# Kernel optimization log

Measured on AMD Instinct MI355X. Metric: run time of the kernel, lower is better.

## Reference

```python
import jax, jax.numpy as jnp
import numpy as np

# Fixed module configuration (matches init_kwargs)
B, T, H, W, C = 2, 16, 32, 32, 512
NH, DH = 8, 64          # num_heads, head_dim = C // NH
MLP = 2048
EPS = 1e-6              # flax LayerNorm default epsilon


def _xavier(key, shape):
    fan_in, fan_out = shape[-2], shape[-1]
    lim = np.sqrt(6.0 / (fan_in + fan_out)).astype(np.float32)
    return jax.random.uniform(key, shape, jnp.float32, -lim, lim)


def setup_inputs() -> dict:
    key = jax.random.key(0)
    ks = jax.random.split(key, 8)
    return {
        "x": jax.random.normal(ks[0], (B, T * H * W, C), jnp.float32),
        # per-axis (stacked: 0=time, 1=height, 2=width) attention params
        "ln_scale": jnp.ones((3, C), jnp.float32),
        "ln_bias": jnp.zeros((3, C), jnp.float32),
        "wq": _xavier(ks[1], (3, C, C)), "bq": jnp.zeros((3, C), jnp.float32),
        "wk": _xavier(ks[2], (3, C, C)), "bk": jnp.zeros((3, C), jnp.float32),
        "wv": _xavier(ks[3], (3, C, C)), "bv": jnp.zeros((3, C), jnp.float32),
        "wo": _xavier(ks[4], (3, C, C)), "bo": jnp.zeros((3, C), jnp.float32),
        # final LN + MLP params
        "ln_mlp_scale": jnp.ones((C,), jnp.float32),
        "ln_mlp_bias": jnp.zeros((C,), jnp.float32),
        "w1": _xavier(ks[5], (C, MLP)),
        "b1": jax.random.normal(ks[6], (MLP,), jnp.float32) * 1e-6,
        "w2": _xavier(ks[7], (MLP, C)),
        "b2": jnp.zeros((C,), jnp.float32),
    }


def _ln(x, scale, bias):
    m = jnp.mean(x, axis=-1, keepdims=True)
    v = jnp.var(x, axis=-1, keepdims=True)
    return (x - m) * jax.lax.rsqrt(v + EPS) * scale + bias


def _mha(x, wq, bq, wk, bk, wv, bv, wo, bo):
    # x: [Bf, S, C]; standard flax-style MHA (query scaled by 1/sqrt(head_dim))
    Bf, S, _ = x.shape
    q = (x @ wq + bq).reshape(Bf, S, NH, DH) * (1.0 / np.sqrt(DH).astype(np.float32))
    k = (x @ wk + bk).reshape(Bf, S, NH, DH)
    v = (x @ wv + bv).reshape(Bf, S, NH, DH)
    a = jax.nn.softmax(jnp.einsum('bqhd,bkhd->bhqk', q, k), axis=-1)
    o = jnp.einsum('bhqk,bkhd->bqhd', a, v).reshape(Bf, S, C)
    return o @ wo + bo


def _axial(x5, axis, sc, bi, wq, bq, wk, bk, wv, bv, wo, bo):
    # fold all non-`axis` spatial dims into batch, attend along `axis`
    other = [a for a in (1, 2, 3) if a != axis]
    perm = [0] + other + [axis, 4]
    xp = jnp.transpose(x5, perm)                      # [..., S_axis, C]
    pshape = xp.shape
    x1 = xp.reshape(-1, pshape[-2], C)                # [Bf, S_axis, C]
    y = _mha(_ln(x1, sc, bi), wq, bq, wk, bk, wv, bv, wo, bo) + x1  # pre-LN residual
    y = y.reshape(pshape)
    inv = list(np.argsort(perm))
    return jnp.transpose(y, inv)


def reference(x, ln_scale, ln_bias, wq, bq, wk, bk, wv, bv, wo, bo,
              ln_mlp_scale, ln_mlp_bias, w1, b1, w2, b2):
    x5 = x.reshape(B, T, H, W, C)
    for i, axis in enumerate((1, 2, 3)):  # time, height, width
        x5 = _axial(x5, axis, ln_scale[i], ln_bias[i], wq[i], bq[i],
                    wk[i], bk[i], wv[i], bv[i], wo[i], bo[i])
    xf = x5.reshape(B, T * H * W, C)
    y = _ln(xf, ln_mlp_scale, ln_mlp_bias)
    y = jax.nn.gelu(y @ w1 + b1) @ w2 + b2            # gelu approximate=True (flax default)
    return xf + y
```

## Files before the change

### kernel.cpp

```cpp
#include <hip/hip_runtime.h>
#include <hip/hip_bf16.h>

typedef __attribute__((ext_vector_type(8))) short short8;
typedef __attribute__((ext_vector_type(4))) float f32x4;

static __device__ __forceinline__ short f2bf(float f) {
    union { __hip_bfloat16 h; short s; } u;
    u.h = __float2bfloat16(f);
    return u.s;
}

static __device__ __forceinline__ float gelu_tanh(float v) {
    const float c = 0.7978845608028654f;
    float t = tanhf(c * (v + 0.044715f * v * v * v));
    return 0.5f * v * (1.f + t);
}

__global__ __launch_bounds__(256) void cvt_weights(
    const float* __restrict__ wq, const float* __restrict__ wk,
    const float* __restrict__ wv, const float* __restrict__ wo,
    const float* __restrict__ w1, const float* __restrict__ w2,
    short* __restrict__ wT)
{
    const long NSQ = 12L * 262144;
    long gid = (long)blockIdx.x * 256 + threadIdx.x;
    if (gid < NSQ) {
        int m = (int)(gid >> 18);
        int rem = (int)(gid & 262143);
        int n = rem >> 9, k = rem & 511;
        int a = m >> 2, t = m & 3;
        const float* src = (t == 0) ? wq : (t == 1) ? wk : (t == 2) ? wv : wo;
        wT[gid] = f2bf(src[(long)a * 262144 + (long)k * 512 + n]);
    } else if (gid < NSQ + 1048576) {
        int r = (int)(gid - NSQ);
        int n = r >> 9, k = r & 511;
        wT[gid] = f2bf(w1[(long)k * 2048 + n]);
    } else {
        int r = (int)(gid - NSQ - 1048576);
        int n = r >> 11, k = r & 2047;
        wT[gid] = f2bf(w2[(long)k * 512 + n]);
    }
}

__global__ __launch_bounds__(256) void ln_kernel(
    const float* __restrict__ x, const float* __restrict__ sc,
    const float* __restrict__ bi, short* __restrict__ out)
{
    int row = blockIdx.x * 4 + (threadIdx.x >> 6);
    int lane = threadIdx.x & 63;
    const float* xr = x + (long)row * 512 + lane * 8;
    f32x4 v0 = *(const f32x4*)xr;
    f32x4 v1 = *(const f32x4*)(xr + 4);
    float s = 0.f, ss = 0.f;
#pragma unroll
    for (int i = 0; i < 4; i++) { s += v0[i] + v1[i]; ss += v0[i] * v0[i] + v1[i] * v1[i]; }
#pragma unroll
    for (int m = 1; m < 64; m <<= 1) { s += __shfl_xor(s, m, 64); ss += __shfl_xor(ss, m, 64); }
    float mean = s * (1.f / 512.f);
    float var  = ss * (1.f / 512.f) - mean * mean;
    float rs = rsqrtf(var + 1e-6f);
    f32x4 s0 = *(const f32x4*)(sc + lane * 8);
    f32x4 s1 = *(const f32x4*)(sc + lane * 8 + 4);
    f32x4 b0 = *(const f32x4*)(bi + lane * 8);
    f32x4 b1 = *(const f32x4*)(bi + lane * 8 + 4);
    short8 o;
#pragma unroll
    for (int i = 0; i < 4; i++) o[i]     = f2bf((v0[i] - mean) * rs * s0[i] + b0[i]);
#pragma unroll
    for (int i = 0; i < 4; i++) o[4 + i] = f2bf((v1[i] - mean) * rs * s1[i] + b1[i]);
    *(short8*)(out + (long)row * 512 + lane * 8) = o;
}

template<int EPI>
__global__ __launch_bounds__(256, 2) void gemm_nt(
    const short* __restrict__ A, const short* __restrict__ Bt,
    const float* __restrict__ bias, const float* __restrict__ bias2,
    const float* __restrict__ bias3,
    const float* __restrict__ res, float* __restrict__ outf,
    short* __restrict__ outb, int M, int N, int K, float scale)
{
    __shared__ __align__(16) short As[128 * 64];
    __shared__ __align__(16) short Bs[128 * 64];
    const int t = threadIdx.x;
    const int lane = t & 63, wid = t >> 6;
    const int wm = wid >> 1, wn = wid & 1;
    const int m0 = blockIdx.x * 128, n0 = blockIdx.y * 128;

    const short* Ag = A  + (long)m0 * K;
    const short* Bg = Bt + (long)n0 * K;

    f32x4 acc[4][4];
#pragma unroll
    for (int i = 0; i < 4; i++)
#pragma unroll
        for (int j = 0; j < 4; j++) acc[i][j] = (f32x4){0.f, 0.f, 0.f, 0.f};

    short8 areg[4], breg[4];
#pragma unroll
    for (int c = 0; c < 4; c++) {
        int g = c * 256 + t; int r = g >> 3, kc = g & 7;
        areg[c] = *(const short8*)(Ag + (long)r * K + kc * 8);
        breg[c] = *(const short8*)(Bg + (long)r * K + kc * 8);
    }
    const int NT = K >> 6;
    for (int tt = 0; tt < NT; ++tt) {
#pragma unroll
        for (int c = 0; c < 4; c++) {
            int g = c * 256 + t; int r = g >> 3, kc = g & 7;
            int off = r * 128 + ((kc * 16) ^ ((r & 7) << 4));
            *(short8*)((char*)As + off) = areg[c];
            *(short8*)((char*)Bs + off) = breg[c];
        }
        __syncthreads();
        if (tt + 1 < NT) {
            const short* Ag2 = Ag + (tt + 1) * 64;
            const short* Bg2 = Bg + (tt + 1) * 64;
#pragma unroll
            for (int c = 0; c < 4; c++) {
                int g = c * 256 + t; int r = g >> 3, kc = g & 7;
                areg[c] = *(const short8*)(Ag2 + (long)r * K + kc * 8);
                breg[c] = *(const short8*)(Bg2 + (long)r * K + kc * 8);
            }
        }
        const int arow = wm * 64 + (lane & 15);
        const int brow = wn * 64 + (lane & 15);
        const int kb = (lane >> 4) * 16;
#pragma unroll
        for (int ks = 0; ks < 2; ++ks) {
            short8 af[4], bfr[4];
#pragma unroll
            for (int f = 0; f < 4; f++) {
                int ra = arow + f * 16;
                af[f]  = *(short8*)((char*)As + ra * 128 + ((kb + ks * 64) ^ ((ra & 7) << 4)));
                int rb = brow + f * 16;
                bfr[f] = *(short8*)((char*)Bs + rb * 128 + ((kb + ks * 64) ^ ((rb & 7) << 4)));
            }
#pragma unroll
            for (int i = 0; i < 4; i++)
#pragma unroll
                for (int j = 0; j < 4; j++)
                    acc[i][j] = __builtin_amdgcn_mfma_f32_16x16x32_bf16(af[i], bfr[j], acc[i][j], 0, 0, 0);
        }
        __syncthreads();
    }

#pragma unroll
    for (int j = 0; j < 4; j++) {
        int col = n0 + wn * 64 + j * 16 + (lane & 15);
        float bv;
        float sc_part = 1.f;
        if (EPI == 3) {
            int part = col >> 9;
            const float* bp = (part == 0) ? bias : (part == 1) ? bias2 : bias3;
            bv = bp[col & 511];
            if (part == 0) sc_part = scale;
        } else {
            bv = bias[col];
        }
#pragma unroll
        for (int i = 0; i < 4; i++) {
            int row0 = m0 + wm * 64 + i * 16 + ((lane >> 4) << 2);
#pragma unroll
            for (int r = 0; r < 4; r++) {
                int row = row0 + r;
                long idx = (long)row * N + col;
                float v = acc[i][j][r] + bv;
                if (EPI == 1)      outf[idx] = v + res[idx];
                else if (EPI == 2) outb[idx] = f2bf(gelu_tanh(v));
                else               outb[idx] = f2bf(v * sc_part);
            }
        }
    }
}

template<int S, int PASS>
__global__ __launch_bounds__(64) void attn_kernel(
    const short* __restrict__ Q, const short* __restrict__ Kx,
    const short* __restrict__ V, short* __restrict__ O, int ld)
{
    constexpr int MF = S / 16;
    constexpr int SP = 32;
    __shared__ __align__(16) short P_lds[S * SP];
    __shared__ __align__(16) short Vt[64 * SP];

    const int lane = threadIdx.x;
    const int pair = blockIdx.x;
    const int head = pair & 7;
    const int bf = pair >> 3;
    long base; int stride;
    if (PASS == 0)      { base = (long)(bf >> 10) * 16384 + (bf & 1023); stride = 1024; }
    else if (PASS == 1) { int b = bf >> 9, t = (bf >> 5) & 15, w = bf & 31; base = (long)b * 16384 + t * 1024 + w; stride = 32; }
    else                { int b = bf >> 9, t = (bf >> 5) & 15, h = bf & 31; base = (long)b * 16384 + t * 1024 + (h << 5); stride = 1; }
    const int hoff = head * 64;

    if (S == 16) {
        short8 z = {0, 0, 0, 0, 0, 0, 0, 0};
        *(short8*)(P_lds + lane * 8) = z;
#pragma unroll
        for (int i = 0; i < 4; i++) *(short8*)(Vt + lane * 32 + i * 8) = z;
        __syncthreads();
    }

    short8 qf[MF][2], kf[MF][2];
#pragma unroll
    for (int f = 0; f < MF; f++) {
        int r = f * 16 + (lane & 15);
        const short* qp = Q + (base + (long)r * stride) * ld + hoff + ((lane >> 4) * 8);
        qf[f][0] = *(const short8*)qp;
        qf[f][1] = *(const short8*)(qp + 32);
        const short* kp = Kx + (base + (long)r * stride) * ld + hoff + ((lane >> 4) * 8);
        kf[f][0] = *(const short8*)kp;
        kf[f][1] = *(const short8*)(kp + 32);
    }

    short8 vv[4];
    const int vr  = (S == 32) ? (lane & 31) : (lane & 15);
    const int vd0 = (S == 32) ? ((lane >> 5) * 32) : ((lane >> 4) * 16);
    constexpr int NVC = (S == 32) ? 4 : 2;
    {
        const short* vp = V + (base + (long)vr * stride) * ld + hoff + vd0;
#pragma unroll
        for (int c = 0; c < NVC; c++) vv[c] = *(const short8*)(vp + c * 8);
    }
#pragma unroll
    for (int c = 0; c < NVC; c++)
#pragma unroll
        for (int e = 0; e < 8; e++)
            Vt[(vd0 + c * 8 + e) * SP + vr] = vv[c][e];

    f32x4 zero4 = {0.f, 0.f, 0.f, 0.f};
    f32x4 sc[MF][MF];
#pragma unroll
    for (int i = 0; i < MF; i++)
#pragma unroll
        for (int j = 0; j < MF; j++) {
            f32x4 a = __builtin_amdgcn_mfma_f32_16x16x32_bf16(qf[i][0], kf[j][0], zero4, 0, 0, 0);
            sc[i][j] = __builtin_amdgcn_mfma_f32_16x16x32_bf16(qf[i][1], kf[j][1], a, 0, 0, 0);
        }

#pragma unroll
    for (int i = 0; i < MF; i++) {
#pragma unroll
        for (int r = 0; r < 4; r++) {
            float mx = sc[i][0][r];
            if (MF == 2) mx = fmaxf(mx, sc[i][1][r]);
#pragma unroll
            for (int m = 1; m < 16; m <<= 1) mx = fmaxf(mx, __shfl_xor(mx, m, 64));
            float e0 = expf(sc[i][0][r] - mx);
            float e1 = (MF == 2) ? expf(sc[i][1][r] - mx) : 0.f;
            float sum = e0 + e1;
#pragma unroll
            for (int m = 1; m < 16; m <<= 1) sum += __shfl_xor(sum, m, 64);
            float inv = 1.f / sum;
            int row = i * 16 + ((lane >> 4) << 2) + r;
            P_lds[row * SP + (lane & 15)] = f2bf(e0 * inv);
            if (MF == 2) P_lds[row * SP + 16 + (lane & 15)] = f2bf(e1 * inv);
        }
    }
    __syncthreads();

    short8 pa[MF];
#pragma unroll
    for (int f = 0; f < MF; f++)
        pa[f] = *(const short8*)(P_lds + (f * 16 + (lane & 15)) * SP + (lane >> 4) * 8);
    short8 vbf[4];
#pragma unroll
    for (int n = 0; n < 4; n++)
        vbf[n] = *(const short8*)(Vt + (n * 16 + (lane & 15)) * SP + (lane >> 4) * 8);
    f32x4 of[MF][4];
#pragma unroll
    for (int f = 0; f < MF; f++)
#pragma unroll
        for (int n = 0; n < 4; n++)
            of[f][n] = __builtin_amdgcn_mfma_f32_16x16x32_bf16(pa[f], vbf[n], zero4, 0, 0, 0);

#pragma unroll
    for (int f = 0; f < MF; f++) {
        int q0 = f * 16 + ((lane >> 4) << 2);
#pragma unroll
        for (int n = 0; n < 4; n++) {
            int d = n * 16 + (lane & 15);
#pragma unroll
            for (int r = 0; r < 4; r++)
                O[(base + (long)(q0 + r) * stride) * 512 + hoff + d] = f2bf(of[f][n][r]);
        }
    }
}

extern "C" void kernel_launch(void* const* d_in, const int* in_sizes, int n_in,
                              void* d_out, int out_size, void* d_ws, size_t ws_size,
                              hipStream_t stream)
{
    const float* x   = (const float*)d_in[0];
    const float* lns = (const float*)d_in[1];
    const float* lnb = (const float*)d_in[2];
    const float* wq  = (const float*)d_in[3];
    const float* bq  = (const float*)d_in[4];
    const float* wk  = (const float*)d_in[5];
    const float* bk  = (const float*)d_in[6];
    const float* wv  = (const float*)d_in[7];
    const float* bv  = (const float*)d_in[8];
    const float* wo  = (const float*)d_in[9];
    const float* bo  = (const float*)d_in[10];
    const float* lms = (const float*)d_in[11];
    const float* lmb = (const float*)d_in[12];
    const float* w1  = (const float*)d_in[13];
    const float* b1  = (const float*)d_in[14];
    const float* w2  = (const float*)d_in[15];
    const float* b2  = (const float*)d_in[16];

    char* ws = (char*)d_ws;
    short* wT   = (short*)ws;
    short* bufA = (short*)(ws + 10485760);
    short* big  = (short*)(ws + 10485760 + 33554432);
    float* xcur = (float*)d_out;

    const int M = 32768;

    cvt_weights<<<20480, 256, 0, stream>>>(wq, wk, wv, wo, w1, w2, wT);

    for (int p = 0; p < 3; ++p) {
        const float* xin = (p == 0) ? x : xcur;
        ln_kernel<<<8192, 256, 0, stream>>>(xin, lns + p * 512, lnb + p * 512, bufA);
        const short* wqkvT = wT + (long)(p * 4) * 262144;
        const short* woT   = wT + (long)(p * 4 + 3) * 262144;
        gemm_nt<3><<<dim3(256, 12), 256, 0, stream>>>(bufA, wqkvT,
            bq + p * 512, bk + p * 512, bv + p * 512,
            nullptr, nullptr, big, M, 1536, 512, 0.125f);
        const short* qb = big, *kb = big + 512, *vbp = big + 1024;
        if (p == 0)      attn_kernel<16, 0><<<16384, 64, 0, stream>>>(qb, kb, vbp, bufA, 1536);
        else if (p == 1) attn_kernel<32, 1><<<8192, 64, 0, stream>>>(qb, kb, vbp, bufA, 1536);
        else             attn_kernel<32, 2><<<8192, 64, 0, stream>>>(qb, kb, vbp, bufA, 1536);
        gemm_nt<1><<<dim3(256, 4), 256, 0, stream>>>(bufA, woT,
            bo + p * 512, nullptr, nullptr, xin, xcur, nullptr, M, 512, 512, 1.f);
    }

    ln_kernel<<<8192, 256, 0, stream>>>(xcur, lms, lmb, bufA);
    const short* w1T = wT + 12L * 262144;
    const short* w2T = wT + 12L * 262144 + 1048576;
    gemm_nt<2><<<dim3(256, 16), 256, 0, stream>>>(bufA, w1T, b1,
        nullptr, nullptr, nullptr, nullptr, big, M, 2048, 512, 1.f);
    gemm_nt<1><<<dim3(256, 4), 256, 0, stream>>>(big, w2T, b2,
        nullptr, nullptr, xcur, xcur, nullptr, M, 512, 2048, 1.f);
}
```

Baseline: 943.7 us.

## Use direct global-to-LDS loads in GEMM and swizzle block order

Replaces the register-staged global loads (with software prefetch of the next tile) by global_load_lds 16-byte direct copies into shared memory, removes the XOR bank swizzle on the LDS layout, and remaps block IDs so that groups of blocks share input tiles in cache. The aim is to save VGPRs and LDS store instructions and improve L2 reuse. In exchange it loses the overlap from register prefetch, since loads are now issued and waited on within the same iteration. The unswizzled LDS reads may also cause bank conflicts, and the block remap assumes the grid size is divisible by 8.

```diff
diff --git a/kernel.cpp b/kernel.cpp
--- a/kernel.cpp
+++ b/kernel.cpp
@@ -14,6 +14,12 @@
     const float c = 0.7978845608028654f;
     float t = tanhf(c * (v + 0.044715f * v * v * v));
     return 0.5f * v * (1.f + t);
+}
+
+static __device__ __forceinline__ void gload16(const void* g, void* l) {
+    __builtin_amdgcn_global_load_lds(
+        (const __attribute__((address_space(1))) void*)g,
+        (__attribute__((address_space(3))) void*)l, 16, 0, 0);
 }
 
 __global__ __launch_bounds__(256) void cvt_weights(
@@ -84,7 +90,12 @@
     const int t = threadIdx.x;
     const int lane = t & 63, wid = t >> 6;
     const int wm = wid >> 1, wn = wid & 1;
-    const int m0 = blockIdx.x * 128, n0 = blockIdx.y * 128;
+
+    const int nbx = gridDim.x;
+    const int bid = blockIdx.y * nbx + blockIdx.x;
+    const int q8 = (nbx * gridDim.y) >> 3;
+    const int swz = (bid & 7) * q8 + (bid >> 3);
+    const int m0 = (swz % nbx) * 128, n0 = (swz / nbx) * 128;
 
     const short* Ag = A  + (long)m0 * K;
     const short* Bg = Bt + (long)n0 * K;
@@ -95,33 +106,20 @@
 #pragma unroll
         for (int j = 0; j < 4; j++) acc[i][j] = (f32x4){0.f, 0.f, 0.f, 0.f};
 
-    short8 areg[4], breg[4];
-#pragma unroll
-    for (int c = 0; c < 4; c++) {
-        int g = c * 256 + t; int r = g >> 3, kc = g & 7;
-        areg[c] = *(const short8*)(Ag + (long)r * K + kc * 8);
-        breg[c] = *(const short8*)(Bg + (long)r * K + kc * 8);
-    }
+    const long rowOff = (long)(t >> 3) * K + (t & 7) * 8;
+    const int  ldsOff = t * 16;
     const int NT = K >> 6;
+
     for (int tt = 0; tt < NT; ++tt) {
+        const short* Asrc = Ag + tt * 64 + rowOff;
+        const short* Bsrc = Bg + tt * 64 + rowOff;
 #pragma unroll
         for (int c = 0; c < 4; c++) {
-            int g = c * 256 + t; int r = g >> 3, kc = g & 7;
-            int off = r * 128 + ((kc * 16) ^ ((r & 7) << 4));
-            *(short8*)((char*)As + off) = areg[c];
-            *(short8*)((char*)Bs + off) = breg[c];
+            gload16(Asrc + (long)c * 32 * K, (char*)As + c * 4096 + ldsOff);
+            gload16(Bsrc + (long)c * 32 * K, (char*)Bs + c * 4096 + ldsOff);
         }
         __syncthreads();
-        if (tt + 1 < NT) {
-            const short* Ag2 = Ag + (tt + 1) * 64;
-            const short* Bg2 = Bg + (tt + 1) * 64;
-#pragma unroll
-            for (int c = 0; c < 4; c++) {
-                int g = c * 256 + t; int r = g >> 3, kc = g & 7;
-                areg[c] = *(const short8*)(Ag2 + (long)r * K + kc * 8);
-                breg[c] = *(const short8*)(Bg2 + (long)r * K + kc * 8);
-            }
-        }
+
         const int arow = wm * 64 + (lane & 15);
         const int brow = wn * 64 + (lane & 15);
         const int kb = (lane >> 4) * 16;
@@ -130,10 +128,8 @@
             short8 af[4], bfr[4];
 #pragma unroll
             for (int f = 0; f < 4; f++) {
-                int ra = arow + f * 16;
-                af[f]  = *(short8*)((char*)As + ra * 128 + ((kb + ks * 64) ^ ((ra & 7) << 4)));
-                int rb = brow + f * 16;
-                bfr[f] = *(short8*)((char*)Bs + rb * 128 + ((kb + ks * 64) ^ ((rb & 7) << 4)));
+                af[f]  = *(short8*)((char*)As + (arow + f * 16) * 128 + kb + ks * 64);
+                bfr[f] = *(short8*)((char*)Bs + (brow + f * 16) * 128 + kb + ks * 64);
             }
 #pragma unroll
             for (int i = 0; i < 4; i++)
```

New measurement: 1.073 ms. 13.7% more time.
